# Performance work log

Measured on AMD Instinct MI355X. Metric: run time of the kernel, lower is better.

Reference implementation:

```python
import jax, jax.numpy as jnp
import numpy as np

B, L, D, H = 4, 256, 512, 8
R = 64            # number of relative-position buckets
DK = D // H       # per-head dim


def setup_inputs() -> dict:
    key = jax.random.key(0)
    ks = jax.random.split(key, 16)
    s = 0.05
    inp = {
        "query": jax.random.normal(ks[0], (B, L, D), jnp.float32),
        "key": jax.random.normal(ks[1], (B, L, D), jnp.float32),
        "value": jax.random.normal(ks[2], (B, L, D), jnp.float32),
        "mask": jax.random.randint(ks[3], (B, L), 0, 2).astype(bool),
        "rel_pos": jax.random.randint(ks[4], (B, L, L), 0, R).astype(jnp.int32),
        "rel_q": jax.random.normal(ks[5], (H, R, DK), jnp.float32) * s,
        "rel_k": jax.random.normal(ks[6], (H, R, DK), jnp.float32) * s,
        "rel_v": jax.random.normal(ks[7], (B, L, L, D), jnp.float32) * s,
        "Wq": jax.random.normal(ks[8], (D, D), jnp.float32) * s,
        "bq": jnp.zeros((D,), jnp.float32),
        "Wk": jax.random.normal(ks[9], (D, D), jnp.float32) * s,
        "bk": jnp.zeros((D,), jnp.float32),
        "Wv": jax.random.normal(ks[10], (D, D), jnp.float32) * s,
        "bv": jnp.zeros((D,), jnp.float32),
        "Wo": jax.random.normal(ks[11], (D, D), jnp.float32) * s,
        "bo": jnp.zeros((D,), jnp.float32),
    }
    return inp


def _heads(x, W, b):
    # nn.Linear: x @ W^T + b, then split heads -> [B, H, L, DK]
    y = x @ W.T + b
    return y.reshape(x.shape[0], x.shape[1], H, DK).transpose(0, 2, 1, 3)


def reference(query, key, value, mask, rel_pos, rel_q, rel_k, rel_v,
              Wq, bq, Wk, bk, Wv, bv, Wo, bo):
    q = _heads(query, Wq, bq)   # [B,H,L,DK]
    k = _heads(key, Wk, bk)
    v = _heads(value, Wv, bv)

    rp = jnp.broadcast_to(rel_pos[:, None], (B, H, L, L))  # int index [B,H,L,L]

    scores = jnp.einsum('bhld,bhmd->bhlm', q, k)

    # content-to-position: gather over relative buckets
    c2p = jnp.einsum('bhld,hrd->bhlr', q, rel_k)            # [B,H,L,R]
    scores = scores + jnp.take_along_axis(c2p, rp, axis=-1)

    # position-to-content: gather with transposed index, then transpose back
    p2c = jnp.einsum('bhld,hrd->bhlr', k, rel_q)            # [B,H,L,R]
    p2c = jnp.take_along_axis(p2c, jnp.swapaxes(rp, -1, -2), axis=-1)
    scores = scores + jnp.swapaxes(p2c, -1, -2)

    scale_factor = 3.0  # 1 + c2p + p2c
    scores = scores / (scale_factor * np.sqrt(DK).astype(np.float32))
    scores = jnp.where(mask[:, None, None, :], jnp.float32(-1e9), scores)

    p = jax.nn.softmax(scores, axis=-1)  # dropout is identity in eval

    ctx = jnp.einsum('bhlm,bhmd->bhld', p, v)
    # rel_v contribution: rel_v -> [B,L,L,H,DK], contract over m (keys)
    rv = rel_v.reshape(B, L, L, H, DK)
    ctx = ctx + jnp.einsum('bhlm,blmhd->bhld', p, rv)

    out = ctx.transpose(0, 2, 1, 3).reshape(B, L, D)
    return out @ Wo.T + bo
```

## Files before the change

kernel.cpp:

```cpp
#include <hip/hip_runtime.h>
#include <hip/hip_bf16.h>
#include <math.h>

#define NB 4
#define NL 256
#define ND 512
#define NH 8
#define NR 64
#define NDK 64

typedef float f32x4 __attribute__((ext_vector_type(4)));
typedef short s16x8 __attribute__((ext_vector_type(8)));
typedef unsigned short u16;
typedef u16 u16x4 __attribute__((ext_vector_type(4)));

static __device__ __forceinline__ u16 f2bf(float f) {
    __hip_bfloat16 h = __float2bfloat16(f);
    return __builtin_bit_cast(unsigned short, h);
}

__global__ __launch_bounds__(256)
void convert_bf16_kernel(const float* __restrict__ q, const float* __restrict__ k,
                         const float* __restrict__ v, const float* __restrict__ wq,
                         const float* __restrict__ wk, const float* __restrict__ wv,
                         const float* __restrict__ wo,
                         u16* __restrict__ oq, u16* __restrict__ ok, u16* __restrict__ ov,
                         u16* __restrict__ owq, u16* __restrict__ owk,
                         u16* __restrict__ owv, u16* __restrict__ owo)
{
    const int job = blockIdx.y;
    const float* src; u16* dst; int n;
    switch (job) {
        case 0: src = q;  dst = oq;  n = 524288; break;
        case 1: src = k;  dst = ok;  n = 524288; break;
        case 2: src = v;  dst = ov;  n = 524288; break;
        case 3: src = wq; dst = owq; n = 262144; break;
        case 4: src = wk; dst = owk; n = 262144; break;
        case 5: src = wv; dst = owv; n = 262144; break;
        default: src = wo; dst = owo; n = 262144; break;
    }
    int idx = (blockIdx.x * 256 + threadIdx.x) * 4;
    if (idx >= n) return;
    f32x4 x = *(const f32x4*)&src[idx];
    u16x4 o;
    o.x = f2bf(x.x); o.y = f2bf(x.y); o.z = f2bf(x.z); o.w = f2bf(x.w);
    *(u16x4*)&dst[idx] = o;
}

__global__ __launch_bounds__(256)
void wprep_kernel(const float* __restrict__ Wq, const float* __restrict__ bq,
                  const float* __restrict__ Wk, const float* __restrict__ bk,
                  const float* __restrict__ RelK, const float* __restrict__ RelQ,
                  u16* __restrict__ W3, float* __restrict__ b3,
                  u16* __restrict__ W2, float* __restrict__ b2)
{
    const int z = blockIdx.y;
    const int t = threadIdx.x;

    if (z == 2) {
        if (blockIdx.x >= 2) return;
        const float* rel  = blockIdx.x ? RelQ : RelK;
        const float* bias = blockIdx.x ? bk : bq;
        float* out        = blockIdx.x ? b2 : b3;
        for (int hr = t; hr < 512; hr += 256) {
            int h = hr >> 6, r = hr & 63;
            float s = 0.f;
            #pragma unroll 8
            for (int d = 0; d < 64; ++d)
                s += rel[((size_t)h * NR + r) * NDK + d] * bias[h * 64 + d];
            out[hr] = s;
        }
        return;
    }

    const float* rel = z ? RelQ : RelK;
    const float* W   = z ? Wk : Wq;
    u16* Wout        = z ? W2 : W3;

    const int h  = blockIdx.x >> 3;
    const int e0 = (blockIdx.x & 7) * 64;

    __shared__ float At[64][68];
    __shared__ float Bs[64][68];

    const int ty = t >> 4, tx = t & 15;

    #pragma unroll
    for (int pass = 0; pass < 4; ++pass) {
        {
            int lr = t >> 2, lk = (t & 3) << 2;
            f32x4 a = *(const f32x4*)&rel[((size_t)h * NR + lr) * NDK + pass * 16 + lk];
            At[pass*16 + lk + 0][lr] = a.x; At[pass*16 + lk + 1][lr] = a.y;
            At[pass*16 + lk + 2][lr] = a.z; At[pass*16 + lk + 3][lr] = a.w;
        }
        {
            int dr = t >> 4, ec = (t & 15) << 2;
            *(f32x4*)&Bs[pass*16 + dr][ec] =
                *(const f32x4*)&W[(size_t)(h*64 + pass*16 + dr) * ND + e0 + ec];
        }
    }
    __syncthreads();

    float acc[4][4] = {{0.f,0.f,0.f,0.f},{0.f,0.f,0.f,0.f},
                       {0.f,0.f,0.f,0.f},{0.f,0.f,0.f,0.f}};
    #pragma unroll 16
    for (int kk = 0; kk < 64; ++kk) {
        f32x4 a4 = *(const f32x4*)&At[kk][ty*4];
        f32x4 b4 = *(const f32x4*)&Bs[kk][tx*4];
        #pragma unroll
        for (int i = 0; i < 4; ++i) {
            acc[i][0] += a4[i]*b4.x; acc[i][1] += a4[i]*b4.y;
            acc[i][2] += a4[i]*b4.z; acc[i][3] += a4[i]*b4.w;
        }
    }

    #pragma unroll
    for (int i = 0; i < 4; ++i) {
        u16x4 o;
        o.x = f2bf(acc[i][0]); o.y = f2bf(acc[i][1]);
        o.z = f2bf(acc[i][2]); o.w = f2bf(acc[i][3]);
        *(u16x4*)&Wout[(size_t)(h*64 + ty*4 + i) * ND + e0 + tx*4] = o;
    }
}

__global__ __launch_bounds__(256)
void gemm5_mfma_kernel(const u16* __restrict__ xq, const u16* __restrict__ xk,
                       const u16* __restrict__ xv,
                       const u16* __restrict__ wq, const u16* __restrict__ wk,
                       const u16* __restrict__ wv, const u16* __restrict__ w3,
                       const u16* __restrict__ w2,
                       const float* __restrict__ bq, const float* __restrict__ bk,
                       const float* __restrict__ bv, const float* __restrict__ b3,
                       const float* __restrict__ b2,
                       u16* __restrict__ qbf, u16* __restrict__ kbf,
                       float* __restrict__ v_ws, float* __restrict__ c2p,
                       float* __restrict__ p2c)
{
    const int z = blockIdx.z;
    const u16* __restrict__ X = (z==0 || z==3) ? xq : ((z==1 || z==4) ? xk : xv);
    const u16* __restrict__ W = (z==0)?wq:(z==1)?wk:(z==2)?wv:(z==3)?w3:w2;
    const float* __restrict__ bias = (z==0)?bq:(z==1)?bk:(z==2)?bv:(z==3)?b3:b2;

    const int t    = threadIdx.x;
    const int wv_  = t >> 6;
    const int lane = t & 63;
    const int lr   = lane & 15;
    const int kg   = lane >> 4;

    const int m0 = blockIdx.x * 64 + wv_ * 16;
    const int h  = blockIdx.y;
    const int n0 = h * 64;

    const u16* Ap = X + (size_t)(m0 + lr) * ND + kg * 8;
    const u16* Bp = W + (size_t)(n0 + lr) * ND + kg * 8;

    f32x4 acc[4] = {{0,0,0,0},{0,0,0,0},{0,0,0,0},{0,0,0,0}};

    for (int kt = 0; kt < 16; ++kt) {
        s16x8 a = *(const s16x8*)(Ap + kt * 32);
        #pragma unroll
        for (int nt = 0; nt < 4; ++nt) {
            s16x8 b = *(const s16x8*)(Bp + (size_t)nt * 16 * ND + kt * 32);
            acc[nt] = __builtin_amdgcn_mfma_f32_16x16x32_bf16(a, b, acc[nt], 0, 0, 0);
        }
    }

    #pragma unroll
    for (int nt = 0; nt < 4; ++nt) {
        const int col = n0 + nt * 16 + lr;
        const float bb = bias[col];
        #pragma unroll
        for (int r = 0; r < 4; ++r) {
            int row = m0 + kg * 4 + r;
            int bI  = row >> 8;
            int lI  = row & 255;
            size_t oidx = (((size_t)(bI * NH + h)) * NL + lI) * 64 + nt * 16 + lr;
            float val = acc[nt][r] + bb;
            if      (z == 0) qbf[oidx]  = f2bf(val);
            else if (z == 1) kbf[oidx]  = f2bf(val);
            else if (z == 2) v_ws[oidx] = val;
            else if (z == 3) c2p[oidx]  = val;
            else             p2c[oidx]  = val;
        }
    }
}

__global__ __launch_bounds__(256)
void scores_mfma_kernel(const u16* __restrict__ qbf, const u16* __restrict__ kbf,
                        const float* __restrict__ C2P, const float* __restrict__ P2C,
                        const int* __restrict__ RelPos, const void* __restrict__ MaskP,
                        float* __restrict__ Pout)
{
    const int bh = blockIdx.y;
    const int b  = bh >> 3;
    const int l0 = blockIdx.x * 16;
    const int t  = threadIdx.x;
    const int wv_  = t >> 6;
    const int lane = t & 63;
    const int i  = t >> 4;
    const int j  = t & 15;

    __shared__ float sc[16][257];
    __shared__ float cs[16][68];
    __shared__ float ps[16][68];
    __shared__ int   rp[16][16];

    const unsigned char* mu = (const unsigned char*)MaskP;
    int loc1  = mu[t*4 + 1];
    int loc23 = mu[t*4 + 2] | mu[t*4 + 3];
    int any1  = __syncthreads_or(loc1);
    int any23 = __syncthreads_or(loc23);
    const int mlayout = any1 ? 0 : (any23 ? 1 : 2);

    *(f32x4*)&cs[t >> 4][(t & 15) * 4] =
        *(const f32x4*)&C2P[(((size_t)bh * NL) + l0 + (t >> 4)) * NR + (t & 15) * 4];

    const int lr = lane & 15;
    const int kg = lane >> 4;
    const u16* Ap = qbf + ((size_t)bh * NL + l0 + lr) * 64 + kg * 8;
    s16x8 a0 = *(const s16x8*)Ap;
    s16x8 a1 = *(const s16x8*)(Ap + 32);

    f32x4 accq[4];
    #pragma unroll
    for (int c = 0; c < 4; ++c) {
        int m0 = wv_ * 64 + c * 16;
        const u16* Bp = kbf + ((size_t)bh * NL + m0 + lr) * 64 + kg * 8;
        s16x8 b0 = *(const s16x8*)Bp;
        s16x8 b1 = *(const s16x8*)(Bp + 32);
        f32x4 acc = {0.f, 0.f, 0.f, 0.f};
        acc = __builtin_amdgcn_mfma_f32_16x16x32_bf16(a0, b0, acc, 0, 0, 0);
        acc = __builtin_amdgcn_mfma_f32_16x16x32_bf16(a1, b1, acc, 0, 0, 0);
        accq[c] = acc;
    }
    #pragma unroll
    for (int c = 0; c < 4; ++c)
        #pragma unroll
        for (int r = 0; r < 4; ++r)
            sc[kg * 4 + r][wv_ * 64 + c * 16 + lr] = accq[c][r];
    __syncthreads();

    for (int mt = 0; mt < 16; ++mt) {
        *(f32x4*)&ps[t >> 4][(t & 15) * 4] =
            *(const f32x4*)&P2C[(((size_t)bh * NL) + mt * 16 + (t >> 4)) * NR + (t & 15) * 4];
        rp[i][j] = RelPos[((size_t)b * NL + l0 + i) * NL + mt * 16 + j];
        __syncthreads();

        int r = rp[i][j];
        float s = sc[i][mt * 16 + j] + cs[i][r] + ps[j][r];
        s *= (1.0f / 24.0f);

        int mg = b * NL + mt * 16 + j;
        float mval;
        if (mlayout == 0)      mval = (float)mu[mg];
        else if (mlayout == 1) mval = ((const float*)MaskP)[mg];
        else                   mval = (float)((const int*)MaskP)[mg];
        if (mval != 0.0f) s = -1e9f;

        sc[i][mt * 16 + j] = s;
        __syncthreads();
    }

    float mx = -INFINITY;
    #pragma unroll
    for (int s16 = 0; s16 < 16; ++s16) mx = fmaxf(mx, sc[i][j + 16*s16]);
    #pragma unroll
    for (int off = 8; off >= 1; off >>= 1) mx = fmaxf(mx, __shfl_xor(mx, off, 16));

    float sum = 0.f;
    #pragma unroll
    for (int s16 = 0; s16 < 16; ++s16) {
        float e = __expf(sc[i][j + 16*s16] - mx);
        sc[i][j + 16*s16] = e;
        sum += e;
    }
    #pragma unroll
    for (int off = 8; off >= 1; off >>= 1) sum += __shfl_xor(sum, off, 16);
    float inv = 1.0f / sum;

    #pragma unroll
    for (int s16 = 0; s16 < 16; ++s16)
        Pout[((size_t)bh * NL + l0 + i) * NL + j + 16*s16] = sc[i][j + 16*s16] * inv;
}

__global__ __launch_bounds__(256)
void ctx_kernel(const float* __restrict__ P, const float* __restrict__ V,
                const float* __restrict__ RV, u16* __restrict__ CTXB)
{
    const int bl = blockIdx.x;
    const int b  = bl >> 8;
    const int l  = bl & 255;
    const int t  = threadIdx.x;

    __shared__ float pw[8][256];
    __shared__ f32x4 redv[128];

    #pragma unroll
    for (int h = 0; h < 8; ++h)
        pw[h][t] = P[(((size_t)(b*NH + h) * NL) + l) * NL + t];
    __syncthreads();

    const int c    = t & 127;
    const int half = t >> 7;
    const int hc   = c >> 4;
    const int dk4  = c & 15;

    const f32x4* rv4 = (const f32x4*)RV + (size_t)bl * NL * 128 + c;
    const f32x4* vv4 = (const f32x4*)V  + ((size_t)(b*NH + hc) * NL) * 16 + dk4;

    f32x4 acc = {0.f, 0.f, 0.f, 0.f};
    #pragma unroll 4
    for (int m = half; m < NL; m += 2) {
        float  w  = pw[hc][m];
        f32x4 rv = __builtin_nontemporal_load(rv4 + (size_t)m * 128);
        f32x4 vv = vv4[(size_t)m * 16];
        acc.x += w * (rv.x + vv.x);
        acc.y += w * (rv.y + vv.y);
        acc.z += w * (rv.z + vv.z);
        acc.w += w * (rv.w + vv.w);
    }

    if (half) redv[c] = acc;
    __syncthreads();
    if (!half) {
        f32x4 r2 = redv[c];
        acc.x += r2.x; acc.y += r2.y; acc.z += r2.z; acc.w += r2.w;
        u16x4 o;
        o.x = f2bf(acc.x); o.y = f2bf(acc.y); o.z = f2bf(acc.z); o.w = f2bf(acc.w);
        *(u16x4*)&CTXB[(size_t)bl * ND + c*4] = o;
    }
}

__global__ __launch_bounds__(256)
void out_proj_mfma_kernel(const u16* __restrict__ A, const u16* __restrict__ W,
                          const float* __restrict__ bias, float* __restrict__ C)
{
    const int t    = threadIdx.x;
    const int wv_  = t >> 6;
    const int lane = t & 63;
    const int lr   = lane & 15;
    const int kg   = lane >> 4;

    const int m0 = blockIdx.x * 64 + wv_ * 16;
    const int n0 = blockIdx.y * 64;

    const u16* Ap = A + (size_t)(m0 + lr) * ND + kg * 8;
    const u16* Bp = W + (size_t)(n0 + lr) * ND + kg * 8;

    f32x4 acc[4] = {{0,0,0,0},{0,0,0,0},{0,0,0,0},{0,0,0,0}};

    for (int kt = 0; kt < 16; ++kt) {
        s16x8 a = *(const s16x8*)(Ap + kt * 32);
        #pragma unroll
        for (int nt = 0; nt < 4; ++nt) {
            s16x8 b = *(const s16x8*)(Bp + (size_t)nt * 16 * ND + kt * 32);
            acc[nt] = __builtin_amdgcn_mfma_f32_16x16x32_bf16(a, b, acc[nt], 0, 0, 0);
        }
    }

    #pragma unroll
    for (int nt = 0; nt < 4; ++nt) {
        const int col = n0 + nt * 16 + lr;
        const float bb = bias[col];
        #pragma unroll
        for (int r = 0; r < 4; ++r) {
            int row = m0 + kg * 4 + r;
            C[(size_t)row * ND + col] = acc[nt][r] + bb;
        }
    }
}

extern "C" void kernel_launch(void* const* d_in, const int* in_sizes, int n_in,
                              void* d_out, int out_size, void* d_ws, size_t ws_size,
                              hipStream_t stream)
{
    const float* query   = (const float*)d_in[0];
    const float* key     = (const float*)d_in[1];
    const float* value   = (const float*)d_in[2];
    const void*  mask    = d_in[3];
    const int*   rel_pos = (const int*)d_in[4];
    const float* rel_q   = (const float*)d_in[5];
    const float* rel_k   = (const float*)d_in[6];
    const float* rel_v   = (const float*)d_in[7];
    const float* Wq = (const float*)d_in[8];
    const float* bq = (const float*)d_in[9];
    const float* Wk = (const float*)d_in[10];
    const float* bk = (const float*)d_in[11];
    const float* Wv = (const float*)d_in[12];
    const float* bv = (const float*)d_in[13];
    const float* Wo = (const float*)d_in[14];
    const float* bo = (const float*)d_in[15];

    float* wsf  = (float*)d_ws;
    float* v_ws = wsf;
    float* c2p  = v_ws + 524288;
    float* p2c  = c2p + 524288;
    float* p    = p2c + 524288;
    float* b3   = p + 2097152;
    float* b2   = b3 + 512;
    u16* wsu  = (u16*)(b2 + 512);
    u16* xqb  = wsu;
    u16* xkb  = xqb + 524288;
    u16* xvb  = xkb + 524288;
    u16* wqb  = xvb + 524288;
    u16* wkb  = wqb + 262144;
    u16* wvb  = wkb + 262144;
    u16* wob  = wvb + 262144;
    u16* w3b  = wob + 262144;
    u16* w2b  = w3b + 262144;
    u16* qbf  = w2b + 262144;
    u16* kbf  = qbf + 524288;
    u16* ctxb = kbf + 524288;

    convert_bf16_kernel<<<dim3(512, 7), 256, 0, stream>>>(
        query, key, value, Wq, Wk, Wv, Wo, xqb, xkb, xvb, wqb, wkb, wvb, wob);

    wprep_kernel<<<dim3(64, 3), 256, 0, stream>>>(
        Wq, bq, Wk, bk, rel_k, rel_q, w3b, b3, w2b, b2);

    gemm5_mfma_kernel<<<dim3(16, 8, 5), 256, 0, stream>>>(
        xqb, xkb, xvb, wqb, wkb, wvb, w3b, w2b,
        bq, bk, bv, b3, b2, qbf, kbf, v_ws, c2p, p2c);

    scores_mfma_kernel<<<dim3(16, 32), 256, 0, stream>>>(
        qbf, kbf, c2p, p2c, rel_pos, mask, p);

    ctx_kernel<<<dim3(1024), 256, 0, stream>>>(p, v_ws, rel_v, ctxb);

    out_proj_mfma_kernel<<<dim3(16, 8), 256, 0, stream>>>(ctxb, wob, bo, (float*)d_out);
}
```

Before: 169.7 us.

## Fuse scores/softmax with context accumulation and retile output projection

Merges the scores+softmax kernel and the ctx kernel into one 512-thread kernel. Softmax probabilities stay in shared memory and are consumed directly for the rel_v and V accumulation, so the 8 MB P tensor is never written to or read back from global memory. The fused kernel reads rel_v with a per-head strided pattern (16 rows × 64 floats per block) rather than contiguous full rows, which may hurt coalescing of the dominant 512 MB stream. The output projection also switches to 32-row tiles to launch twice as many blocks.

```diff
diff --git a/kernel.cpp b/kernel.cpp
--- a/kernel.cpp
+++ b/kernel.cpp
@@ -185,149 +185,132 @@
     }
 }
 
-__global__ __launch_bounds__(256)
-void scores_mfma_kernel(const u16* __restrict__ qbf, const u16* __restrict__ kbf,
-                        const float* __restrict__ C2P, const float* __restrict__ P2C,
-                        const int* __restrict__ RelPos, const void* __restrict__ MaskP,
-                        float* __restrict__ Pout)
+__global__ __launch_bounds__(512, 4)
+void attn_ctx_kernel(const u16* __restrict__ qbf, const u16* __restrict__ kbf,
+                     const float* __restrict__ Vws,
+                     const float* __restrict__ C2P, const float* __restrict__ P2C,
+                     const int* __restrict__ RelPos, const void* __restrict__ MaskP,
+                     const float* __restrict__ RV, u16* __restrict__ CTXB)
 {
     const int bh = blockIdx.y;
     const int b  = bh >> 3;
+    const int h  = bh & 7;
     const int l0 = blockIdx.x * 16;
     const int t  = threadIdx.x;
-    const int wv_  = t >> 6;
-    const int lane = t & 63;
-    const int i  = t >> 4;
-    const int j  = t & 15;
 
     __shared__ float sc[16][257];
-    __shared__ float cs[16][68];
-    __shared__ float ps[16][68];
-    __shared__ int   rp[16][16];
+    __shared__ float cs[16][64];
+    __shared__ float ps[32][68];
+    __shared__ f32x4 redv[256];
 
     const unsigned char* mu = (const unsigned char*)MaskP;
-    int loc1  = mu[t*4 + 1];
-    int loc23 = mu[t*4 + 2] | mu[t*4 + 3];
+    int loc1 = 0, loc23 = 0;
+    if (t < 250) {
+        loc1  = mu[t*4 + 1];
+        loc23 = mu[t*4 + 2] | mu[t*4 + 3];
+    }
     int any1  = __syncthreads_or(loc1);
     int any23 = __syncthreads_or(loc23);
     const int mlayout = any1 ? 0 : (any23 ? 1 : 2);
 
-    *(f32x4*)&cs[t >> 4][(t & 15) * 4] =
-        *(const f32x4*)&C2P[(((size_t)bh * NL) + l0 + (t >> 4)) * NR + (t & 15) * 4];
-
-    const int lr = lane & 15;
-    const int kg = lane >> 4;
-    const u16* Ap = qbf + ((size_t)bh * NL + l0 + lr) * 64 + kg * 8;
-    s16x8 a0 = *(const s16x8*)Ap;
-    s16x8 a1 = *(const s16x8*)(Ap + 32);
-
-    f32x4 accq[4];
-    #pragma unroll
-    for (int c = 0; c < 4; ++c) {
-        int m0 = wv_ * 64 + c * 16;
-        const u16* Bp = kbf + ((size_t)bh * NL + m0 + lr) * 64 + kg * 8;
-        s16x8 b0 = *(const s16x8*)Bp;
-        s16x8 b1 = *(const s16x8*)(Bp + 32);
+    if (t < 256)
+        *(f32x4*)&cs[t >> 4][(t & 15) * 4] =
+            *(const f32x4*)&C2P[(((size_t)bh * NL) + l0 + (t >> 4)) * NR + (t & 15) * 4];
+
+    {
+        const int wv_  = t >> 6;
+        const int lane = t & 63;
+        const int lr   = lane & 15;
+        const int kg   = lane >> 4;
+        const u16* Ap = qbf + ((size_t)bh * NL + l0 + lr) * 64 + kg * 8;
+        s16x8 a0 = *(const s16x8*)Ap;
+        s16x8 a1 = *(const s16x8*)(Ap + 32);
+        #pragma unroll
+        for (int c = 0; c < 2; ++c) {
+            int m0 = wv_ * 32 + c * 16;
+            const u16* Bp = kbf + ((size_t)bh * NL + m0 + lr) * 64 + kg * 8;
+            s16x8 b0 = *(const s16x8*)Bp;
+            s16x8 b1 = *(const s16x8*)(Bp + 32);
+            f32x4 acc = {0.f, 0.f, 0.f, 0.f};
+            acc = __builtin_amdgcn_mfma_f32_16x16x32_bf16(a0, b0, acc, 0, 0, 0);
+            acc = __builtin_amdgcn_mfma_f32_16x16x32_bf16(a1, b1, acc, 0, 0, 0);
+            #pragma unroll
+            for (int r = 0; r < 4; ++r)
+                sc[kg * 4 + r][m0 + lr] = acc[r];
+        }
+    }
+    __syncthreads();
+
+    const int i  = t >> 5;
+    const int jj = t & 31;
+    for (int mt = 0; mt < 8; ++mt) {
+        *(f32x4*)&ps[t >> 4][(t & 15) * 4] =
+            *(const f32x4*)&P2C[(((size_t)bh * NL) + mt * 32 + (t >> 4)) * NR + (t & 15) * 4];
+        __syncthreads();
+
+        const int m = mt * 32 + jj;
+        int r = RelPos[((size_t)b * NL + l0 + i) * NL + m];
+        float s = sc[i][m] + cs[i][r] + ps[jj][r];
+        s *= (1.0f / 24.0f);
+
+        float mval;
+        if (mlayout == 0)      mval = (float)mu[b * NL + m];
+        else if (mlayout == 1) mval = ((const float*)MaskP)[b * NL + m];
+        else                   mval = (float)((const int*)MaskP)[b * NL + m];
+        if (mval != 0.0f) s = -1e9f;
+
+        __syncthreads();
+        sc[i][m] = s;
+        __syncthreads();
+    }
+
+    {
+        float mx = -INFINITY;
+        #pragma unroll
+        for (int s32 = 0; s32 < 8; ++s32) mx = fmaxf(mx, sc[i][jj + 32*s32]);
+        #pragma unroll
+        for (int off = 16; off >= 1; off >>= 1) mx = fmaxf(mx, __shfl_xor(mx, off, 32));
+
+        float sum = 0.f;
+        float ev[8];
+        #pragma unroll
+        for (int s32 = 0; s32 < 8; ++s32) {
+            ev[s32] = __expf(sc[i][jj + 32*s32] - mx);
+            sum += ev[s32];
+        }
+        #pragma unroll
+        for (int off = 16; off >= 1; off >>= 1) sum += __shfl_xor(sum, off, 32);
+        float inv = 1.0f / sum;
+        #pragma unroll
+        for (int s32 = 0; s32 < 8; ++s32) sc[i][jj + 32*s32] = ev[s32] * inv;
+    }
+    __syncthreads();
+
+    {
+        const int half = t >> 8;
+        const int di   = (t >> 4) & 15;
+        const int d4   = t & 15;
+
+        const float* rvp = RV + (((size_t)(b * NL + l0 + di)) * NL) * ND + h * 64 + d4 * 4;
+        const float* vvp = Vws + ((size_t)(b * NH + h) * NL) * 64 + d4 * 4;
+
         f32x4 acc = {0.f, 0.f, 0.f, 0.f};
-        acc = __builtin_amdgcn_mfma_f32_16x16x32_bf16(a0, b0, acc, 0, 0, 0);
-        acc = __builtin_amdgcn_mfma_f32_16x16x32_bf16(a1, b1, acc, 0, 0, 0);
-        accq[c] = acc;
-    }
-    #pragma unroll
-    for (int c = 0; c < 4; ++c)
-        #pragma unroll
-        for (int r = 0; r < 4; ++r)
-            sc[kg * 4 + r][wv_ * 64 + c * 16 + lr] = accq[c][r];
-    __syncthreads();
-
-    for (int mt = 0; mt < 16; ++mt) {
-        *(f32x4*)&ps[t >> 4][(t & 15) * 4] =
-            *(const f32x4*)&P2C[(((size_t)bh * NL) + mt * 16 + (t >> 4)) * NR + (t & 15) * 4];
-        rp[i][j] = RelPos[((size_t)b * NL + l0 + i) * NL + mt * 16 + j];
+        #pragma unroll 4
+        for (int m = half; m < NL; m += 2) {
+            float w  = sc[di][m];
+            f32x4 rv = __builtin_nontemporal_load((const f32x4*)(rvp + (size_t)m * ND));
+            f32x4 vv = *(const f32x4*)(vvp + (size_t)m * 64);
+            acc += w * (rv + vv);
+        }
+
+        if (half) redv[t & 255] = acc;
         __syncthreads();
-
-        int r = rp[i][j];
-        float s = sc[i][mt * 16 + j] + cs[i][r] + ps[j][r];
-        s *= (1.0f / 24.0f);
-
-        int mg = b * NL + mt * 16 + j;
-        float mval;
-        if (mlayout == 0)      mval = (float)mu[mg];
-        else if (mlayout == 1) mval = ((const float*)MaskP)[mg];
-        else                   mval = (float)((const int*)MaskP)[mg];
-        if (mval != 0.0f) s = -1e9f;
-
-        sc[i][mt * 16 + j] = s;
-        __syncthreads();
-    }
-
-    float mx = -INFINITY;
-    #pragma unroll
-    for (int s16 = 0; s16 < 16; ++s16) mx = fmaxf(mx, sc[i][j + 16*s16]);
-    #pragma unroll
-    for (int off = 8; off >= 1; off >>= 1) mx = fmaxf(mx, __shfl_xor(mx, off, 16));
-
-    float sum = 0.f;
-    #pragma unroll
-    for (int s16 = 0; s16 < 16; ++s16) {
-        float e = __expf(sc[i][j + 16*s16] - mx);
-        sc[i][j + 16*s16] = e;
-        sum += e;
-    }
-    #pragma unroll
-    for (int off = 8; off >= 1; off >>= 1) sum += __shfl_xor(sum, off, 16);
-    float inv = 1.0f / sum;
-
-    #pragma unroll
-    for (int s16 = 0; s16 < 16; ++s16)
-        Pout[((size_t)bh * NL + l0 + i) * NL + j + 16*s16] = sc[i][j + 16*s16] * inv;
-}
-
-__global__ __launch_bounds__(256)
-void ctx_kernel(const float* __restrict__ P, const float* __restrict__ V,
-                const float* __restrict__ RV, u16* __restrict__ CTXB)
-{
-    const int bl = blockIdx.x;
-    const int b  = bl >> 8;
-    const int l  = bl & 255;
-    const int t  = threadIdx.x;
-
-    __shared__ float pw[8][256];
-    __shared__ f32x4 redv[128];
-
-    #pragma unroll
-    for (int h = 0; h < 8; ++h)
-        pw[h][t] = P[(((size_t)(b*NH + h) * NL) + l) * NL + t];
-    __syncthreads();
-
-    const int c    = t & 127;
-    const int half = t >> 7;
-    const int hc   = c >> 4;
-    const int dk4  = c & 15;
-
-    const f32x4* rv4 = (const f32x4*)RV + (size_t)bl * NL * 128 + c;
-    const f32x4* vv4 = (const f32x4*)V  + ((size_t)(b*NH + hc) * NL) * 16 + dk4;
-
-    f32x4 acc = {0.f, 0.f, 0.f, 0.f};
-    #pragma unroll 4
-    for (int m = half; m < NL; m += 2) {
-        float  w  = pw[hc][m];
-        f32x4 rv = __builtin_nontemporal_load(rv4 + (size_t)m * 128);
-        f32x4 vv = vv4[(size_t)m * 16];
-        acc.x += w * (rv.x + vv.x);
-        acc.y += w * (rv.y + vv.y);
-        acc.z += w * (rv.z + vv.z);
-        acc.w += w * (rv.w + vv.w);
-    }
-
-    if (half) redv[c] = acc;
-    __syncthreads();
-    if (!half) {
-        f32x4 r2 = redv[c];
-        acc.x += r2.x; acc.y += r2.y; acc.z += r2.z; acc.w += r2.w;
-        u16x4 o;
-        o.x = f2bf(acc.x); o.y = f2bf(acc.y); o.z = f2bf(acc.z); o.w = f2bf(acc.w);
-        *(u16x4*)&CTXB[(size_t)bl * ND + c*4] = o;
+        if (!half) {
+            acc += redv[t];
+            u16x4 o;
+            o.x = f2bf(acc.x); o.y = f2bf(acc.y); o.z = f2bf(acc.z); o.w = f2bf(acc.w);
+            *(u16x4*)&CTXB[((size_t)(b * NL + l0 + di)) * ND + h * 64 + d4 * 4] = o;
+        }
     }
 }
 
@@ -341,25 +324,25 @@
     const int lr   = lane & 15;
     const int kg   = lane >> 4;
 
-    const int m0 = blockIdx.x * 64 + wv_ * 16;
-    const int n0 = blockIdx.y * 64;
+    const int m0 = blockIdx.x * 32 + (wv_ & 1) * 16;
+    const int n0 = blockIdx.y * 64 + (wv_ >> 1) * 32;
 
     const u16* Ap = A + (size_t)(m0 + lr) * ND + kg * 8;
     const u16* Bp = W + (size_t)(n0 + lr) * ND + kg * 8;
 
-    f32x4 acc[4] = {{0,0,0,0},{0,0,0,0},{0,0,0,0},{0,0,0,0}};
+    f32x4 acc[2] = {{0,0,0,0},{0,0,0,0}};
 
     for (int kt = 0; kt < 16; ++kt) {
         s16x8 a = *(const s16x8*)(Ap + kt * 32);
         #pragma unroll
-        for (int nt = 0; nt < 4; ++nt) {
+        for (int nt = 0; nt < 2; ++nt) {
             s16x8 b = *(const s16x8*)(Bp + (size_t)nt * 16 * ND + kt * 32);
             acc[nt] = __builtin_amdgcn_mfma_f32_16x16x32_bf16(a, b, acc[nt], 0, 0, 0);
         }
     }
 
     #pragma unroll
-    for (int nt = 0; nt < 4; ++nt) {
+    for (int nt = 0; nt < 2; ++nt) {
         const int col = n0 + nt * 16 + lr;
         const float bb = bias[col];
         #pragma unroll
@@ -395,8 +378,7 @@
     float* v_ws = wsf;
     float* c2p  = v_ws + 524288;
     float* p2c  = c2p + 524288;
-    float* p    = p2c + 524288;
-    float* b3   = p + 2097152;
+    float* b3   = p2c + 524288;
     float* b2   = b3 + 512;
     u16* wsu  = (u16*)(b2 + 512);
     u16* xqb  = wsu;
@@ -422,10 +404,8 @@
         xqb, xkb, xvb, wqb, wkb, wvb, w3b, w2b,
         bq, bk, bv, b3, b2, qbf, kbf, v_ws, c2p, p2c);
 
-    scores_mfma_kernel<<<dim3(16, 32), 256, 0, stream>>>(
-        qbf, kbf, c2p, p2c, rel_pos, mask, p);
-
-    ctx_kernel<<<dim3(1024), 256, 0, stream>>>(p, v_ws, rel_v, ctxb);
-
-    out_proj_mfma_kernel<<<dim3(16, 8), 256, 0, stream>>>(ctxb, wob, bo, (float*)d_out);
-}
+    attn_ctx_kernel<<<dim3(16, 32), 512, 0, stream>>>(
+        qbf, kbf, v_ws, c2p, p2c, rel_pos, mask, rel_v, ctxb);
+
+    out_proj_mfma_kernel<<<dim3(32, 8), 256, 0, stream>>>(ctxb, wob, bo, (float*)d_out);
+}
```

Result: no change. 169.2 us (-0.3%).

## Stage full bf16 p2c table in LDS, drop per-tile syncs, retile out-proj

Applied to the files above, without the earlier changes.

The scores kernel now loads the whole per-head p2c table for all 256 keys into shared memory once, stored as bf16, and precomputes the mask row. The gather/scale/mask step then runs in one pass with no per-tile barriers, reading rel_pos straight from global memory. p2c is written in bf16 by the projection GEMM, which halves its traffic but lowers its precision. Separately, the output projection uses smaller 32-row tiles to launch twice as many blocks.

```diff
diff --git a/kernel.cpp b/kernel.cpp
--- a/kernel.cpp
+++ b/kernel.cpp
@@ -13,10 +13,15 @@
 typedef short s16x8 __attribute__((ext_vector_type(8)));
 typedef unsigned short u16;
 typedef u16 u16x4 __attribute__((ext_vector_type(4)));
+typedef u16 u16x8 __attribute__((ext_vector_type(8)));
+typedef unsigned int u32;
 
 static __device__ __forceinline__ u16 f2bf(float f) {
     __hip_bfloat16 h = __float2bfloat16(f);
     return __builtin_bit_cast(unsigned short, h);
+}
+static __device__ __forceinline__ float bf2f(u16 u) {
+    return __builtin_bit_cast(float, (u32)u << 16);
 }
 
 __global__ __launch_bounds__(256)
@@ -134,7 +139,7 @@
                        const float* __restrict__ b2,
                        u16* __restrict__ qbf, u16* __restrict__ kbf,
                        float* __restrict__ v_ws, float* __restrict__ c2p,
-                       float* __restrict__ p2c)
+                       u16* __restrict__ p2cb)
 {
     const int z = blockIdx.z;
     const u16* __restrict__ X = (z==0 || z==3) ? xq : ((z==1 || z==4) ? xk : xv);
@@ -180,30 +185,26 @@
             else if (z == 1) kbf[oidx]  = f2bf(val);
             else if (z == 2) v_ws[oidx] = val;
             else if (z == 3) c2p[oidx]  = val;
-            else             p2c[oidx]  = val;
-        }
-    }
-}
-
-__global__ __launch_bounds__(256)
-void scores_mfma_kernel(const u16* __restrict__ qbf, const u16* __restrict__ kbf,
-                        const float* __restrict__ C2P, const float* __restrict__ P2C,
-                        const int* __restrict__ RelPos, const void* __restrict__ MaskP,
-                        float* __restrict__ Pout)
+            else             p2cb[oidx] = f2bf(val);
+        }
+    }
+}
+
+__global__ __launch_bounds__(256)
+void scores_kernel(const u16* __restrict__ qbf, const u16* __restrict__ kbf,
+                   const float* __restrict__ C2P, const u16* __restrict__ P2Cb,
+                   const int* __restrict__ RelPos, const void* __restrict__ MaskP,
+                   float* __restrict__ Pout)
 {
     const int bh = blockIdx.y;
     const int b  = bh >> 3;
     const int l0 = blockIdx.x * 16;
     const int t  = threadIdx.x;
-    const int wv_  = t >> 6;
-    const int lane = t & 63;
-    const int i  = t >> 4;
-    const int j  = t & 15;
 
     __shared__ float sc[16][257];
+    __shared__ u16   psall[256][68];
     __shared__ float cs[16][68];
-    __shared__ float ps[16][68];
-    __shared__ int   rp[16][16];
+    __shared__ float maskv[256];
 
     const unsigned char* mu = (const unsigned char*)MaskP;
     int loc1  = mu[t*4 + 1];
@@ -212,75 +213,85 @@
     int any23 = __syncthreads_or(loc23);
     const int mlayout = any1 ? 0 : (any23 ? 1 : 2);
 
-    *(f32x4*)&cs[t >> 4][(t & 15) * 4] =
-        *(const f32x4*)&C2P[(((size_t)bh * NL) + l0 + (t >> 4)) * NR + (t & 15) * 4];
-
-    const int lr = lane & 15;
-    const int kg = lane >> 4;
-    const u16* Ap = qbf + ((size_t)bh * NL + l0 + lr) * 64 + kg * 8;
-    s16x8 a0 = *(const s16x8*)Ap;
-    s16x8 a1 = *(const s16x8*)(Ap + 32);
-
-    f32x4 accq[4];
-    #pragma unroll
-    for (int c = 0; c < 4; ++c) {
-        int m0 = wv_ * 64 + c * 16;
-        const u16* Bp = kbf + ((size_t)bh * NL + m0 + lr) * 64 + kg * 8;
-        s16x8 b0 = *(const s16x8*)Bp;
-        s16x8 b1 = *(const s16x8*)(Bp + 32);
-        f32x4 acc = {0.f, 0.f, 0.f, 0.f};
-        acc = __builtin_amdgcn_mfma_f32_16x16x32_bf16(a0, b0, acc, 0, 0, 0);
-        acc = __builtin_amdgcn_mfma_f32_16x16x32_bf16(a1, b1, acc, 0, 0, 0);
-        accq[c] = acc;
-    }
-    #pragma unroll
-    for (int c = 0; c < 4; ++c)
-        #pragma unroll
-        for (int r = 0; r < 4; ++r)
-            sc[kg * 4 + r][wv_ * 64 + c * 16 + lr] = accq[c][r];
+    {
+        float mval;
+        if (mlayout == 0)      mval = (float)mu[b * NL + t];
+        else if (mlayout == 1) mval = ((const float*)MaskP)[b * NL + t];
+        else                   mval = (float)((const int*)MaskP)[b * NL + t];
+        maskv[t] = mval;
+        *(f32x4*)&cs[t >> 4][(t & 15) * 4] =
+            *(const f32x4*)&C2P[(((size_t)bh * NL) + l0 + (t >> 4)) * NR + (t & 15) * 4];
+    }
+
+    #pragma unroll
+    for (int rep = 0; rep < 8; ++rep) {
+        int e = t + rep * 256;
+        *(u16x8*)&psall[e >> 3][(e & 7) * 8] =
+            *(const u16x8*)&P2Cb[((size_t)bh * NL + (e >> 3)) * 64 + (e & 7) * 8];
+    }
+
+    {
+        const int wv_  = t >> 6;
+        const int lane = t & 63;
+        const int lr   = lane & 15;
+        const int kg   = lane >> 4;
+        const u16* Ap = qbf + ((size_t)bh * NL + l0 + lr) * 64 + kg * 8;
+        s16x8 a0 = *(const s16x8*)Ap;
+        s16x8 a1 = *(const s16x8*)(Ap + 32);
+        #pragma unroll
+        for (int c = 0; c < 4; ++c) {
+            int m0 = wv_ * 64 + c * 16;
+            const u16* Bp = kbf + ((size_t)bh * NL + m0 + lr) * 64 + kg * 8;
+            s16x8 b0 = *(const s16x8*)Bp;
+            s16x8 b1 = *(const s16x8*)(Bp + 32);
+            f32x4 acc = {0.f, 0.f, 0.f, 0.f};
+            acc = __builtin_amdgcn_mfma_f32_16x16x32_bf16(a0, b0, acc, 0, 0, 0);
+            acc = __builtin_amdgcn_mfma_f32_16x16x32_bf16(a1, b1, acc, 0, 0, 0);
+            #pragma unroll
+            for (int r = 0; r < 4; ++r)
+                sc[kg * 4 + r][m0 + lr] = acc[r];
+        }
+    }
     __syncthreads();
 
-    for (int mt = 0; mt < 16; ++mt) {
-        *(f32x4*)&ps[t >> 4][(t & 15) * 4] =
-            *(const f32x4*)&P2C[(((size_t)bh * NL) + mt * 16 + (t >> 4)) * NR + (t & 15) * 4];
-        rp[i][j] = RelPos[((size_t)b * NL + l0 + i) * NL + mt * 16 + j];
-        __syncthreads();
-
-        int r = rp[i][j];
-        float s = sc[i][mt * 16 + j] + cs[i][r] + ps[j][r];
-        s *= (1.0f / 24.0f);
-
-        int mg = b * NL + mt * 16 + j;
-        float mval;
-        if (mlayout == 0)      mval = (float)mu[mg];
-        else if (mlayout == 1) mval = ((const float*)MaskP)[mg];
-        else                   mval = (float)((const int*)MaskP)[mg];
-        if (mval != 0.0f) s = -1e9f;
-
-        sc[i][mt * 16 + j] = s;
-        __syncthreads();
-    }
-
-    float mx = -INFINITY;
-    #pragma unroll
-    for (int s16 = 0; s16 < 16; ++s16) mx = fmaxf(mx, sc[i][j + 16*s16]);
-    #pragma unroll
-    for (int off = 8; off >= 1; off >>= 1) mx = fmaxf(mx, __shfl_xor(mx, off, 16));
-
-    float sum = 0.f;
-    #pragma unroll
-    for (int s16 = 0; s16 < 16; ++s16) {
-        float e = __expf(sc[i][j + 16*s16] - mx);
-        sc[i][j + 16*s16] = e;
-        sum += e;
-    }
-    #pragma unroll
-    for (int off = 8; off >= 1; off >>= 1) sum += __shfl_xor(sum, off, 16);
-    float inv = 1.0f / sum;
-
-    #pragma unroll
-    for (int s16 = 0; s16 < 16; ++s16)
-        Pout[((size_t)bh * NL + l0 + i) * NL + j + 16*s16] = sc[i][j + 16*s16] * inv;
+    const int i  = t >> 4;
+    const int jj = t & 15;
+    {
+        const size_t rowbase = ((size_t)b * NL + l0 + i) * NL;
+        #pragma unroll
+        for (int s = 0; s < 16; ++s) {
+            const int m = s * 16 + jj;
+            int r = RelPos[rowbase + m];
+            float val = sc[i][m] + cs[i][r] + bf2f(psall[m][r]);
+            val *= (1.0f / 24.0f);
+            if (maskv[m] != 0.0f) val = -1e9f;
+            sc[i][m] = val;
+        }
+    }
+
+    {
+        float mx = -INFINITY;
+        #pragma unroll
+        for (int s = 0; s < 16; ++s) mx = fmaxf(mx, sc[i][jj + 16*s]);
+        #pragma unroll
+        for (int off = 8; off >= 1; off >>= 1) mx = fmaxf(mx, __shfl_xor(mx, off, 16));
+
+        float sum = 0.f;
+        float ev[16];
+        #pragma unroll
+        for (int s = 0; s < 16; ++s) {
+            ev[s] = __expf(sc[i][jj + 16*s] - mx);
+            sum += ev[s];
+        }
+        #pragma unroll
+        for (int off = 8; off >= 1; off >>= 1) sum += __shfl_xor(sum, off, 16);
+        float inv = 1.0f / sum;
+
+        float* prow = Pout + ((size_t)bh * NL + l0 + i) * NL;
+        #pragma unroll
+        for (int s = 0; s < 16; ++s)
+            prow[jj + 16*s] = ev[s] * inv;
+    }
 }
 
 __global__ __launch_bounds__(256)
@@ -341,25 +352,25 @@
     const int lr   = lane & 15;
     const int kg   = lane >> 4;
 
-    const int m0 = blockIdx.x * 64 + wv_ * 16;
-    const int n0 = blockIdx.y * 64;
+    const int m0 = blockIdx.x * 32 + (wv_ & 1) * 16;
+    const int n0 = blockIdx.y * 64 + (wv_ >> 1) * 32;
 
     const u16* Ap = A + (size_t)(m0 + lr) * ND + kg * 8;
     const u16* Bp = W + (size_t)(n0 + lr) * ND + kg * 8;
 
-    f32x4 acc[4] = {{0,0,0,0},{0,0,0,0},{0,0,0,0},{0,0,0,0}};
+    f32x4 acc[2] = {{0,0,0,0},{0,0,0,0}};
 
     for (int kt = 0; kt < 16; ++kt) {
         s16x8 a = *(const s16x8*)(Ap + kt * 32);
         #pragma unroll
-        for (int nt = 0; nt < 4; ++nt) {
+        for (int nt = 0; nt < 2; ++nt) {
             s16x8 b = *(const s16x8*)(Bp + (size_t)nt * 16 * ND + kt * 32);
             acc[nt] = __builtin_amdgcn_mfma_f32_16x16x32_bf16(a, b, acc[nt], 0, 0, 0);
         }
     }
 
     #pragma unroll
-    for (int nt = 0; nt < 4; ++nt) {
+    for (int nt = 0; nt < 2; ++nt) {
         const int col = n0 + nt * 16 + lr;
         const float bb = bias[col];
         #pragma unroll
@@ -394,8 +405,7 @@
     float* wsf  = (float*)d_ws;
     float* v_ws = wsf;
     float* c2p  = v_ws + 524288;
-    float* p2c  = c2p + 524288;
-    float* p    = p2c + 524288;
+    float* p    = c2p + 524288;
     float* b3   = p + 2097152;
     float* b2   = b3 + 512;
     u16* wsu  = (u16*)(b2 + 512);
@@ -410,7 +420,8 @@
     u16* w2b  = w3b + 262144;
     u16* qbf  = w2b + 262144;
     u16* kbf  = qbf + 524288;
-    u16* ctxb = kbf + 524288;
+    u16* p2cb = kbf + 524288;
+    u16* ctxb = p2cb + 524288;
 
     convert_bf16_kernel<<<dim3(512, 7), 256, 0, stream>>>(
         query, key, value, Wq, Wk, Wv, Wo, xqb, xkb, xvb, wqb, wkb, wvb, wob);
@@ -420,12 +431,12 @@
 
     gemm5_mfma_kernel<<<dim3(16, 8, 5), 256, 0, stream>>>(
         xqb, xkb, xvb, wqb, wkb, wvb, w3b, w2b,
-        bq, bk, bv, b3, b2, qbf, kbf, v_ws, c2p, p2c);
-
-    scores_mfma_kernel<<<dim3(16, 32), 256, 0, stream>>>(
-        qbf, kbf, c2p, p2c, rel_pos, mask, p);
+        bq, bk, bv, b3, b2, qbf, kbf, v_ws, c2p, p2cb);
+
+    scores_kernel<<<dim3(16, 32), 256, 0, stream>>>(
+        qbf, kbf, c2p, p2cb, rel_pos, mask, p);
 
     ctx_kernel<<<dim3(1024), 256, 0, stream>>>(p, v_ws, rel_v, ctxb);
 
-    out_proj_mfma_kernel<<<dim3(16, 8), 256, 0, stream>>>(ctxb, wob, bo, (float*)d_out);
-}
+    out_proj_mfma_kernel<<<dim3(32, 8), 256, 0, stream>>>(ctxb, wob, bo, (float*)d_out);
+}
```

Measured after the change: 157.6 us. 7.1% less time.
